# Kernel tuning notes

Measured on AMD Instinct MI355X. Metric: run time of the kernel, lower is better.

Reference implementation:

```python
import jax, jax.numpy as jnp
import numpy as np
import math

B, LQ, LK, DK, DV, H = 8, 2048, 2048, 128, 128, 8

def setup_inputs() -> dict:
    key = jax.random.key(0)
    ks = jax.random.split(key, 8)
    s = 0.02  # weight init scale
    return {
        "q": jax.random.normal(ks[0], (B, LQ, DK), jnp.float32),
        "k": jax.random.normal(ks[1], (B, LK, DK), jnp.float32),
        "v": jax.random.normal(ks[2], (B, LK, DV), jnp.float32),
        "Wq": jax.random.normal(ks[3], (DK, H * DK), jnp.float32) * s,
        "bq": jnp.zeros((H * DK,), jnp.float32),
        "Wk": jax.random.normal(ks[4], (DK, H * DK), jnp.float32) * s,
        "bk": jnp.zeros((H * DK,), jnp.float32),
        "Wv": jax.random.normal(ks[5], (DV, H * DV), jnp.float32) * s,
        "bv": jnp.zeros((H * DV,), jnp.float32),
        "Wo": jax.random.normal(ks[6], (H * DV, DV), jnp.float32) * s,
        "bo": jnp.zeros((DV,), jnp.float32),
    }

def reference(q, k, v, Wq, bq, Wk, bk, Wv, bv, Wo, bo):
    b, lq, dk = q.shape
    lk = k.shape[1]
    h = Wq.shape[1] // dk
    dv = Wv.shape[0]
    # projections -> [B, L, H, d]
    Qh = (q @ Wq + bq).reshape(b, lq, h, dk)
    Kh = (k @ Wk + bk).reshape(b, lk, h, dk)
    Vh = (v @ Wv + bv).reshape(b, lk, h, dv)
    scale = 1.0 / math.sqrt(dk)
    # full attention scores [B, H, Lq, Lk]
    scores = jnp.einsum("bqhd,bkhd->bhqk", Qh, Kh) * scale
    attn = jax.nn.softmax(scores, axis=-1)
    # dropout=0.0 in eval mode -> no-op
    out = jnp.einsum("bhqk,bkhd->bqhd", attn, Vh).reshape(b, lq, h * dv)
    return out @ Wo + bo  # [B, Lq, d_v]
```

## Files before the change

### kernel.cpp

```cpp
#include <hip/hip_runtime.h>
#include <hip/hip_bf16.h>
#include <math.h>


typedef __attribute__((ext_vector_type(8))) short s16x8;
typedef __attribute__((ext_vector_type(4))) short s16x4;
typedef __attribute__((ext_vector_type(4))) float f32x4;

#define MFMA16(a, b, c) __builtin_amdgcn_mfma_f32_16x16x32_bf16((a), (b), (c), 0, 0, 0)

static constexpr int HN = 8, LN = 2048;
static constexpr int MROWS = 16384;

static __device__ __forceinline__ unsigned short f2b(float f) {
  __hip_bfloat16 h = __float2bfloat16(f);
  union { __hip_bfloat16 h; unsigned short u; } cv;
  cv.h = h;
  return cv.u;
}

static __device__ __forceinline__ s16x8 ld16(const void* p) {
  uint4 t = *(const uint4*)p;
  return __builtin_bit_cast(s16x8, t);
}

static __device__ __forceinline__ void gload16(const void* g, void* l) {
  __builtin_amdgcn_global_load_lds(
      (const __attribute__((address_space(1))) unsigned int*)g,
      (__attribute__((address_space(3))) unsigned int*)l, 16, 0, 0);
}

static __device__ __forceinline__ unsigned cvt_pk(float lo, float hi) {
  unsigned r;
  asm("v_cvt_pk_bf16_f32 %0, %1, %2" : "=v"(r) : "v"(lo), "v"(hi));
  return r;
}

static __device__ __forceinline__ float fexp2(float x) {
  float r;
  asm("v_exp_f32 %0, %1" : "=v"(r) : "v"(x));
  return r;
}

__global__ __launch_bounds__(256) void cast_kernel(
    const float* __restrict__ q, const float* __restrict__ k,
    const float* __restrict__ v, const float* __restrict__ Wq,
    const float* __restrict__ Wk, const float* __restrict__ Wv,
    const float* __restrict__ Wo,
    __hip_bfloat16* __restrict__ qb, __hip_bfloat16* __restrict__ kb,
    __hip_bfloat16* __restrict__ vb, __hip_bfloat16* __restrict__ Wqt,
    __hip_bfloat16* __restrict__ Wkt, __hip_bfloat16* __restrict__ Wvt,
    __hip_bfloat16* __restrict__ Wot, float qscale)
{
  const int bid = blockIdx.x, tid = threadIdx.x;
  if (bid < 6144) {
    const int idx4 = bid * 256 + tid;
    const int arr  = idx4 >> 19;
    const int off4 = idx4 & ((1 << 19) - 1);
    const float* src = (arr == 0) ? q : (arr == 1) ? k : v;
    __hip_bfloat16* dst = (arr == 0) ? qb : (arr == 1) ? kb : vb;
    float4 ld = ((const float4*)src)[off4];
    s16x4 pk;
    pk[0] = (short)f2b(ld.x); pk[1] = (short)f2b(ld.y);
    pk[2] = (short)f2b(ld.z); pk[3] = (short)f2b(ld.w);
    ((s16x4*)dst)[off4] = pk;
  } else {
    const int t = (bid - 6144) * 256 + tid;
    const int which = t >> 17;
    const int i = t & ((1 << 17) - 1);
    if (which < 3) {
      const int n = i >> 7, kk = i & 127;
      const float* W = (which == 0) ? Wq : (which == 1) ? Wk : Wv;
      __hip_bfloat16* Wt = (which == 0) ? Wqt : (which == 1) ? Wkt : Wvt;
      float val = W[kk * 1024 + n];
      if (which == 0) val *= qscale;
      Wt[n * 128 + kk] = __float2bfloat16(val);
    } else {
      const int n = i >> 10, kk = i & 1023;
      Wot[n * 1024 + kk] = __float2bfloat16(Wo[kk * 128 + n]);
    }
  }
}

template <int MODE, int NF>
__global__ __launch_bounds__(256) void gemm_kernel(
    const __hip_bfloat16* __restrict__ A, const __hip_bfloat16* __restrict__ Btr,
    const float* __restrict__ bias, void* __restrict__ outp,
    int K, float bias_scale)
{
  constexpr int BUFB = (4 + NF) * 4096;
  __shared__ char lds[2 * BUFB];

  const int tid = threadIdx.x;
  const int l = tid & 63, w = tid >> 6;
  const int wr = w >> 1, wc = w & 1;
  const int m0 = blockIdx.x * 128, n0 = blockIdx.y * (NF * 32);
  const int cq = l & 15, rg = l >> 4;
  const int lrow8 = l >> 3, lcol8 = l & 7;
  const int swz8 = (lcol8 ^ lrow8) * 8;
  const int nk = K >> 6;

  f32x4 acc[4][NF] = {};

  auto stage = [&](int bb, int k0) {
    char* Ab = lds + bb * BUFB;
    char* Bb = Ab + 16384;
#pragma unroll
    for (int c = 0; c < 4; ++c) {
      const int ca = w * 4 + c;
      gload16(A + (size_t)(m0 + ca * 8 + lrow8) * K + k0 + swz8, Ab + ca * 1024);
    }
#pragma unroll
    for (int c = 0; c < NF; ++c) {
      const int cb = w * NF + c;
      gload16(Btr + (size_t)(n0 + cb * 8 + lrow8) * K + k0 + swz8, Bb + cb * 1024);
    }
  };

  stage(0, 0);
  __syncthreads();

  for (int kt = 0; kt < nk; ++kt) {
    const int cur = kt & 1;
    if (kt + 1 < nk) stage(cur ^ 1, (kt + 1) << 6);
    char* As = lds + cur * BUFB;
    char* Bs = As + 16384;
#pragma unroll
    for (int ks = 0; ks < 2; ++ks) {
      s16x8 af[4], bf[NF];
#pragma unroll
      for (int mf = 0; mf < 4; ++mf) {
        const int arow = wr * 64 + mf * 16 + cq;
        af[mf] = ld16(As + arow * 128 + ((ks * 64 + rg * 16) ^ ((arow & 7) << 4)));
      }
#pragma unroll
      for (int nf = 0; nf < NF; ++nf) {
        const int brow = wc * (NF * 16) + nf * 16 + cq;
        bf[nf] = ld16(Bs + brow * 128 + ((ks * 64 + rg * 16) ^ ((brow & 7) << 4)));
      }
#pragma unroll
      for (int mf = 0; mf < 4; ++mf)
#pragma unroll
        for (int nf = 0; nf < NF; ++nf)
          acc[mf][nf] = MFMA16(af[mf], bf[nf], acc[mf][nf]);
    }
    __syncthreads();
  }

#pragma unroll
  for (int nf = 0; nf < NF; ++nf) {
    const int gn = n0 + wc * (NF * 16) + nf * 16 + cq;
    const float bv = bias[gn] * bias_scale;
#pragma unroll
    for (int mf = 0; mf < 4; ++mf) {
      const int gm0 = m0 + wr * 64 + mf * 16 + rg * 4;
      const f32x4 a = acc[mf][nf];
      if (MODE == 0) {
        const int h = gn >> 7, d = gn & 127;
        __hip_bfloat16* o = (__hip_bfloat16*)outp;
#pragma unroll
        for (int r = 0; r < 4; ++r) {
          const int gm = gm0 + r;
          const int b = gm >> 11, lr = gm & (LN - 1);
          o[((size_t)(b * HN + h) * LN + lr) * 128 + d] = __float2bfloat16(a[r] + bv);
        }
      } else if (MODE == 2) {
        const int h = gn >> 7, d = gn & 127;
        const int b = gm0 >> 11, kv = gm0 & (LN - 1);
        s16x4 pk;
#pragma unroll
        for (int r = 0; r < 4; ++r) pk[r] = (short)f2b(a[r] + bv);
        *(s16x4*)((__hip_bfloat16*)outp + ((size_t)(b * HN + h) * 128 + d) * LN + kv) = pk;
      } else {
        float* o = (float*)outp;
#pragma unroll
        for (int r = 0; r < 4; ++r)
          o[(size_t)(gm0 + r) * 128 + gn] = a[r] + bv;
      }
    }
  }
}

__global__ __launch_bounds__(256, 2) void attn_kernel(
    const __hip_bfloat16* __restrict__ Qh, const __hip_bfloat16* __restrict__ Kh,
    const __hip_bfloat16* __restrict__ Vt, __hip_bfloat16* __restrict__ Obuf)
{
  __shared__ char lds[73728];
  char* Ks = lds;
  char* Vs = lds + 32768;

  const int x = blockIdx.x;
  const int xcd = x & 7, ii = x >> 3;
  const int bh = xcd * 8 + (ii >> 4);
  const int qt = ii & 15;

  const int tid = threadIdx.x, l = tid & 63, w = tid >> 6;
  const int cq = l & 15, rg = l >> 4;
  const int q0 = qt * 128 + w * 32;

  char* Pw = lds + 65536 + w * 2048;

  const char* Qc = (const char*)(Qh + (size_t)bh * LN * 128);
  const char* Kc = (const char*)(Kh + (size_t)bh * LN * 128);
  const char* Vc = (const char*)(Vt + (size_t)bh * 128 * LN);

  s16x8 qreg[2][4];
#pragma unroll
  for (int qf = 0; qf < 2; ++qf)
#pragma unroll
    for (int ks = 0; ks < 4; ++ks)
      qreg[qf][ks] = ld16(Qc + (size_t)(q0 + qf * 16 + cq) * 256 + ks * 64 + rg * 16);

  int kgoff[4], vgoff[4];
#pragma unroll
  for (int j = 0; j < 4; ++j) {
    const int ck = w * 256 + j * 64 + l;
    const int kr = ck >> 4, kc = ck & 15;
    kgoff[j] = kr * 256 + ((kc ^ (kr & 7)) * 16);
    const int vr = ck >> 3, vc = ck & 7;
    vgoff[j] = vr * 4096 + ((vc ^ (vr & 7)) * 16);
  }

  auto stageKV = [&](int buf, int t) {
    const char* kg = Kc + (size_t)t * 16384;
    const char* vg = Vc + (size_t)t * 128;
#pragma unroll
    for (int j = 0; j < 4; ++j) {
      gload16(kg + kgoff[j], Ks + buf * 16384 + w * 4096 + j * 1024);
      gload16(vg + vgoff[j], Vs + buf * 16384 + w * 4096 + j * 1024);
    }
  };

  f32x4 acc[8][2] = {};
  float ls0 = 0.f, ls1 = 0.f;

  stageKV(0, 0);
  __syncthreads();

#pragma unroll 2
  for (int t = 0; t < 32; ++t) {
    const int cur = t & 1;
    if (t < 31) stageKV(cur ^ 1, t + 1);
    char* Kb = Ks + cur * 16384;
    char* Vb = Vs + cur * 16384;

    f32x4 st[2][4] = {};
    __builtin_amdgcn_s_setprio(1);
#pragma unroll
    for (int t4 = 0; t4 < 4; ++t4) {
      const int row = t4 * 16 + cq;
      const int rsw = (row & 7) << 4;
      s16x8 kf[4];
#pragma unroll
      for (int ks = 0; ks < 4; ++ks)
        kf[ks] = ld16(Kb + row * 256 + ((ks * 64 + rg * 16) ^ rsw));
#pragma unroll
      for (int ks = 0; ks < 4; ++ks) {
        st[0][t4] = MFMA16(kf[ks], qreg[0][ks], st[0][t4]);
        st[1][t4] = MFMA16(kf[ks], qreg[1][ks], st[1][t4]);
      }
    }
    __builtin_amdgcn_s_setprio(0);

    s16x8 pb[2][2];
#pragma unroll
    for (int qf = 0; qf < 2; ++qf) {
      float sum = 0.f;
      const int prow = cq * 128;
      const int psw = (cq & 7) << 4;
#pragma unroll
      for (int t4 = 0; t4 < 4; ++t4) {
        const float e0 = fexp2(st[qf][t4][0]);
        const float e1 = fexp2(st[qf][t4][1]);
        const float e2 = fexp2(st[qf][t4][2]);
        const float e3 = fexp2(st[qf][t4][3]);
        sum += (e0 + e1) + (e2 + e3);
        uint2 pk;
        pk.x = cvt_pk(e0, e1);
        pk.y = cvt_pk(e2, e3);
        *(uint2*)(Pw + prow + ((t4 * 32 + rg * 8) ^ psw)) = pk;
      }
      if (qf) ls1 += sum; else ls0 += sum;
      pb[qf][0] = ld16(Pw + prow + ((rg * 16) ^ psw));
      pb[qf][1] = ld16(Pw + prow + ((64 + rg * 16) ^ psw));
    }

    __builtin_amdgcn_s_setprio(1);
#pragma unroll
    for (int fd = 0; fd < 8; ++fd) {
      const int vrow = fd * 16 + cq;
      const int vsw = (vrow & 7) << 4;
      s16x8 va0 = ld16(Vb + vrow * 128 + ((rg * 16) ^ vsw));
      s16x8 va1 = ld16(Vb + vrow * 128 + ((64 + rg * 16) ^ vsw));
      acc[fd][0] = MFMA16(va0, pb[0][0], acc[fd][0]);
      acc[fd][0] = MFMA16(va1, pb[0][1], acc[fd][0]);
      acc[fd][1] = MFMA16(va0, pb[1][0], acc[fd][1]);
      acc[fd][1] = MFMA16(va1, pb[1][1], acc[fd][1]);
    }
    __builtin_amdgcn_s_setprio(0);

    __syncthreads();
  }

  ls0 += __shfl_xor(ls0, 16); ls0 += __shfl_xor(ls0, 32);
  ls1 += __shfl_xor(ls1, 16); ls1 += __shfl_xor(ls1, 32);
  const float ri0 = 1.0f / ls0, ri1 = 1.0f / ls1;

  char* Ow = lds + w * 8192;
#pragma unroll
  for (int fd = 0; fd < 8; ++fd)
#pragma unroll
    for (int qf = 0; qf < 2; ++qf) {
      const float ri = qf ? ri1 : ri0;
      const int ql = qf * 16 + cq;
#pragma unroll
      for (int rr = 0; rr < 4; rr += 2) {
        const unsigned int pk = (unsigned)f2b(acc[fd][qf][rr] * ri) |
                                ((unsigned)f2b(acc[fd][qf][rr + 1] * ri) << 16);
        const int d0 = fd * 16 + rg * 4 + rr;
        *(unsigned int*)(Ow + ql * 256 + ((d0 * 2) ^ ((ql & 7) << 4))) = pk;
      }
    }
  const int b = bh >> 3, h = bh & 7;
#pragma unroll
  for (int pr = 0; pr < 8; ++pr) {
    const int ql = pr * 4 + rg;
    uint4 ov = *(const uint4*)(Ow + ql * 256 + ((cq * 16) ^ ((ql & 7) << 4)));
    *(uint4*)((char*)Obuf + ((size_t)(b * LN + q0 + ql) * 1024 + h * 128) * 2 + cq * 16) = ov;
  }
}

extern "C" void kernel_launch(void* const* d_in, const int* in_sizes, int n_in,
                              void* d_out, int out_size, void* d_ws, size_t ws_size,
                              hipStream_t stream)
{
  (void)in_sizes; (void)n_in; (void)out_size; (void)ws_size;
  const float* q  = (const float*)d_in[0];
  const float* k  = (const float*)d_in[1];
  const float* v  = (const float*)d_in[2];
  const float* Wq = (const float*)d_in[3];
  const float* bq = (const float*)d_in[4];
  const float* Wk = (const float*)d_in[5];
  const float* bk = (const float*)d_in[6];
  const float* Wv = (const float*)d_in[7];
  const float* bv = (const float*)d_in[8];
  const float* Wo = (const float*)d_in[9];
  const float* bo = (const float*)d_in[10];

  char* ws = (char*)d_ws;
  size_t off = 0;
  auto alloc = [&](size_t bytes) { char* p = ws + off; off += (bytes + 255) & ~(size_t)255; return p; };
  __hip_bfloat16* qb  = (__hip_bfloat16*)alloc((size_t)MROWS * 128 * 2);
  __hip_bfloat16* kb  = (__hip_bfloat16*)alloc((size_t)MROWS * 128 * 2);
  __hip_bfloat16* vb  = (__hip_bfloat16*)alloc((size_t)MROWS * 128 * 2);
  __hip_bfloat16* Wqt = (__hip_bfloat16*)alloc(1024 * 128 * 2);
  __hip_bfloat16* Wkt = (__hip_bfloat16*)alloc(1024 * 128 * 2);
  __hip_bfloat16* Wvt = (__hip_bfloat16*)alloc(1024 * 128 * 2);
  __hip_bfloat16* Wot = (__hip_bfloat16*)alloc(128 * 1024 * 2);
  __hip_bfloat16* Qh  = (__hip_bfloat16*)alloc((size_t)64 * LN * 128 * 2);
  __hip_bfloat16* Kh  = (__hip_bfloat16*)alloc((size_t)64 * LN * 128 * 2);
  __hip_bfloat16* Vt  = (__hip_bfloat16*)alloc((size_t)64 * LN * 128 * 2);
  __hip_bfloat16* Ob  = (__hip_bfloat16*)alloc((size_t)MROWS * 1024 * 2);

  const float qscale = 1.4426950408889634f / sqrtf(128.0f);

  cast_kernel<<<8192, 256, 0, stream>>>(q, k, v, Wq, Wk, Wv, Wo,
                                        qb, kb, vb, Wqt, Wkt, Wvt, Wot, qscale);
  gemm_kernel<0, 4><<<dim3(128, 8), 256, 0, stream>>>(qb, Wqt, bq, Qh, 128, qscale);
  gemm_kernel<0, 4><<<dim3(128, 8), 256, 0, stream>>>(kb, Wkt, bk, Kh, 128, 1.0f);
  gemm_kernel<2, 4><<<dim3(128, 8), 256, 0, stream>>>(vb, Wvt, bv, Vt, 128, 1.0f);
  attn_kernel<<<1024, 256, 0, stream>>>(Qh, Kh, Vt, Ob);
  gemm_kernel<3, 2><<<dim3(128, 2), 256, 0, stream>>>(Ob, Wot, bo, d_out, 1024, 1.0f);
}
```

Measured before the change: 216.3 us.

## Double attention Q tile per wave to 64 rows, halving grid

```diff
diff --git a/kernel.cpp b/kernel.cpp
--- a/kernel.cpp
+++ b/kernel.cpp
@@ -181,32 +181,32 @@
   }
 }
 
-__global__ __launch_bounds__(256, 2) void attn_kernel(
+__global__ __launch_bounds__(256, 1) void attn_kernel(
     const __hip_bfloat16* __restrict__ Qh, const __hip_bfloat16* __restrict__ Kh,
     const __hip_bfloat16* __restrict__ Vt, __hip_bfloat16* __restrict__ Obuf)
 {
-  __shared__ char lds[73728];
+  __shared__ char lds[98304];
   char* Ks = lds;
   char* Vs = lds + 32768;
 
   const int x = blockIdx.x;
   const int xcd = x & 7, ii = x >> 3;
-  const int bh = xcd * 8 + (ii >> 4);
-  const int qt = ii & 15;
+  const int bh = xcd * 8 + (ii >> 3);
+  const int qt = ii & 7;
 
   const int tid = threadIdx.x, l = tid & 63, w = tid >> 6;
   const int cq = l & 15, rg = l >> 4;
-  const int q0 = qt * 128 + w * 32;
-
-  char* Pw = lds + 65536 + w * 2048;
+  const int q0 = qt * 256 + w * 64;
+
+  char* Pw = lds + 65536 + w * 8192;
 
   const char* Qc = (const char*)(Qh + (size_t)bh * LN * 128);
   const char* Kc = (const char*)(Kh + (size_t)bh * LN * 128);
   const char* Vc = (const char*)(Vt + (size_t)bh * 128 * LN);
 
-  s16x8 qreg[2][4];
-#pragma unroll
-  for (int qf = 0; qf < 2; ++qf)
+  s16x8 qreg[4][4];
+#pragma unroll
+  for (int qf = 0; qf < 4; ++qf)
 #pragma unroll
     for (int ks = 0; ks < 4; ++ks)
       qreg[qf][ks] = ld16(Qc + (size_t)(q0 + qf * 16 + cq) * 256 + ks * 64 + rg * 16);
@@ -231,20 +231,21 @@
     }
   };
 
-  f32x4 acc[8][2] = {};
-  float ls0 = 0.f, ls1 = 0.f;
+  f32x4 acc[8][4] = {};
+  float ls[4] = {0.f, 0.f, 0.f, 0.f};
 
   stageKV(0, 0);
   __syncthreads();
 
-#pragma unroll 2
+  const int psw = (cq & 7) << 4;
+
   for (int t = 0; t < 32; ++t) {
     const int cur = t & 1;
     if (t < 31) stageKV(cur ^ 1, t + 1);
     char* Kb = Ks + cur * 16384;
     char* Vb = Vs + cur * 16384;
 
-    f32x4 st[2][4] = {};
+    f32x4 st[4][4] = {};
     __builtin_amdgcn_s_setprio(1);
 #pragma unroll
     for (int t4 = 0; t4 < 4; ++t4) {
@@ -255,19 +256,17 @@
       for (int ks = 0; ks < 4; ++ks)
         kf[ks] = ld16(Kb + row * 256 + ((ks * 64 + rg * 16) ^ rsw));
 #pragma unroll
-      for (int ks = 0; ks < 4; ++ks) {
-        st[0][t4] = MFMA16(kf[ks], qreg[0][ks], st[0][t4]);
-        st[1][t4] = MFMA16(kf[ks], qreg[1][ks], st[1][t4]);
-      }
+      for (int ks = 0; ks < 4; ++ks)
+#pragma unroll
+        for (int qf = 0; qf < 4; ++qf)
+          st[qf][t4] = MFMA16(kf[ks], qreg[qf][ks], st[qf][t4]);
     }
     __builtin_amdgcn_s_setprio(0);
 
-    s16x8 pb[2][2];
-#pragma unroll
-    for (int qf = 0; qf < 2; ++qf) {
+#pragma unroll
+    for (int qf = 0; qf < 4; ++qf) {
+      const int prow = (qf * 16 + cq) * 128;
       float sum = 0.f;
-      const int prow = cq * 128;
-      const int psw = (cq & 7) << 4;
 #pragma unroll
       for (int t4 = 0; t4 < 4; ++t4) {
         const float e0 = fexp2(st[qf][t4][0]);
@@ -280,7 +279,12 @@
         pk.y = cvt_pk(e2, e3);
         *(uint2*)(Pw + prow + ((t4 * 32 + rg * 8) ^ psw)) = pk;
       }
-      if (qf) ls1 += sum; else ls0 += sum;
+      ls[qf] += sum;
+    }
+    s16x8 pb[4][2];
+#pragma unroll
+    for (int qf = 0; qf < 4; ++qf) {
+      const int prow = (qf * 16 + cq) * 128;
       pb[qf][0] = ld16(Pw + prow + ((rg * 16) ^ psw));
       pb[qf][1] = ld16(Pw + prow + ((64 + rg * 16) ^ psw));
     }
@@ -292,38 +296,42 @@
       const int vsw = (vrow & 7) << 4;
       s16x8 va0 = ld16(Vb + vrow * 128 + ((rg * 16) ^ vsw));
       s16x8 va1 = ld16(Vb + vrow * 128 + ((64 + rg * 16) ^ vsw));
-      acc[fd][0] = MFMA16(va0, pb[0][0], acc[fd][0]);
-      acc[fd][0] = MFMA16(va1, pb[0][1], acc[fd][0]);
-      acc[fd][1] = MFMA16(va0, pb[1][0], acc[fd][1]);
-      acc[fd][1] = MFMA16(va1, pb[1][1], acc[fd][1]);
+#pragma unroll
+      for (int qf = 0; qf < 4; ++qf) {
+        acc[fd][qf] = MFMA16(va0, pb[qf][0], acc[fd][qf]);
+        acc[fd][qf] = MFMA16(va1, pb[qf][1], acc[fd][qf]);
+      }
     }
     __builtin_amdgcn_s_setprio(0);
 
     __syncthreads();
   }
 
-  ls0 += __shfl_xor(ls0, 16); ls0 += __shfl_xor(ls0, 32);
-  ls1 += __shfl_xor(ls1, 16); ls1 += __shfl_xor(ls1, 32);
-  const float ri0 = 1.0f / ls0, ri1 = 1.0f / ls1;
-
-  char* Ow = lds + w * 8192;
+  float ri[4];
+#pragma unroll
+  for (int qf = 0; qf < 4; ++qf) {
+    float s = ls[qf];
+    s += __shfl_xor(s, 16); s += __shfl_xor(s, 32);
+    ri[qf] = 1.0f / s;
+  }
+
+  char* Ow = lds + w * 16384;
 #pragma unroll
   for (int fd = 0; fd < 8; ++fd)
 #pragma unroll
-    for (int qf = 0; qf < 2; ++qf) {
-      const float ri = qf ? ri1 : ri0;
+    for (int qf = 0; qf < 4; ++qf) {
       const int ql = qf * 16 + cq;
 #pragma unroll
       for (int rr = 0; rr < 4; rr += 2) {
-        const unsigned int pk = (unsigned)f2b(acc[fd][qf][rr] * ri) |
-                                ((unsigned)f2b(acc[fd][qf][rr + 1] * ri) << 16);
+        const unsigned int pk = (unsigned)f2b(acc[fd][qf][rr] * ri[qf]) |
+                                ((unsigned)f2b(acc[fd][qf][rr + 1] * ri[qf]) << 16);
         const int d0 = fd * 16 + rg * 4 + rr;
         *(unsigned int*)(Ow + ql * 256 + ((d0 * 2) ^ ((ql & 7) << 4))) = pk;
       }
     }
   const int b = bh >> 3, h = bh & 7;
 #pragma unroll
-  for (int pr = 0; pr < 8; ++pr) {
+  for (int pr = 0; pr < 16; ++pr) {
     const int ql = pr * 4 + rg;
     uint4 ov = *(const uint4*)(Ow + ql * 256 + ((cq * 16) ^ ((ql & 7) << 4)));
     *(uint4*)((char*)Obuf + ((size_t)(b * LN + q0 + ql) * 1024 + h * 128) * 2 + cq * 16) = ov;
@@ -369,6 +377,6 @@
   gemm_kernel<0, 4><<<dim3(128, 8), 256, 0, stream>>>(qb, Wqt, bq, Qh, 128, qscale);
   gemm_kernel<0, 4><<<dim3(128, 8), 256, 0, stream>>>(kb, Wkt, bk, Kh, 128, 1.0f);
   gemm_kernel<2, 4><<<dim3(128, 8), 256, 0, stream>>>(vb, Wvt, bv, Vt, 128, 1.0f);
-  attn_kernel<<<1024, 256, 0, stream>>>(Qh, Kh, Vt, Ob);
+  attn_kernel<<<512, 256, 0, stream>>>(Qh, Kh, Vt, Ob);
   gemm_kernel<3, 2><<<dim3(128, 2), 256, 0, stream>>>(Ob, Wot, bo, d_out, 1024, 1.0f);
 }
```

Measured after the change: 266.8 us. 23.3% more time.

## Halve attention KV tile to 32 keys to shrink LDS footprint

Applied to the files above, without the earlier changes.

```diff
diff --git a/kernel.cpp b/kernel.cpp
--- a/kernel.cpp
+++ b/kernel.cpp
@@ -185,9 +185,9 @@
     const __hip_bfloat16* __restrict__ Qh, const __hip_bfloat16* __restrict__ Kh,
     const __hip_bfloat16* __restrict__ Vt, __hip_bfloat16* __restrict__ Obuf)
 {
-  __shared__ char lds[73728];
+  __shared__ char lds[40960];
   char* Ks = lds;
-  char* Vs = lds + 32768;
+  char* Vs = lds + 16384;
 
   const int x = blockIdx.x;
   const int xcd = x & 7, ii = x >> 3;
@@ -198,7 +198,7 @@
   const int cq = l & 15, rg = l >> 4;
   const int q0 = qt * 128 + w * 32;
 
-  char* Pw = lds + 65536 + w * 2048;
+  char* Pw = lds + 32768 + w * 2048;
 
   const char* Qc = (const char*)(Qh + (size_t)bh * LN * 128);
   const char* Kc = (const char*)(Kh + (size_t)bh * LN * 128);
@@ -211,23 +211,26 @@
     for (int ks = 0; ks < 4; ++ks)
       qreg[qf][ks] = ld16(Qc + (size_t)(q0 + qf * 16 + cq) * 256 + ks * 64 + rg * 16);
 
-  int kgoff[4], vgoff[4];
-#pragma unroll
-  for (int j = 0; j < 4; ++j) {
-    const int ck = w * 256 + j * 64 + l;
+  int kgoff[2], vgoff[2];
+#pragma unroll
+  for (int j = 0; j < 2; ++j) {
+    const int ck = w * 128 + j * 64 + l;
     const int kr = ck >> 4, kc = ck & 15;
     kgoff[j] = kr * 256 + ((kc ^ (kr & 7)) * 16);
-    const int vr = ck >> 3, vc = ck & 7;
-    vgoff[j] = vr * 4096 + ((vc ^ (vr & 7)) * 16);
+    const int vr = ck >> 3, vsl = ck & 7;
+    const int s2 = vsl ^ (vr & 7);
+    const int d  = vr * 2 + (s2 >> 2);
+    const int kvc = s2 & 3;
+    vgoff[j] = d * 4096 + kvc * 16;
   }
 
   auto stageKV = [&](int buf, int t) {
-    const char* kg = Kc + (size_t)t * 16384;
-    const char* vg = Vc + (size_t)t * 128;
-#pragma unroll
-    for (int j = 0; j < 4; ++j) {
-      gload16(kg + kgoff[j], Ks + buf * 16384 + w * 4096 + j * 1024);
-      gload16(vg + vgoff[j], Vs + buf * 16384 + w * 4096 + j * 1024);
+    const char* kg = Kc + (size_t)t * 8192;
+    const char* vg = Vc + (size_t)t * 64;
+#pragma unroll
+    for (int j = 0; j < 2; ++j) {
+      gload16(kg + kgoff[j], Ks + buf * 8192 + w * 2048 + j * 1024);
+      gload16(vg + vgoff[j], Vs + buf * 8192 + w * 2048 + j * 1024);
     }
   };
 
@@ -237,17 +240,18 @@
   stageKV(0, 0);
   __syncthreads();
 
-#pragma unroll 2
-  for (int t = 0; t < 32; ++t) {
+  const int cqs = cq & 3;
+
+  for (int t = 0; t < 64; ++t) {
     const int cur = t & 1;
-    if (t < 31) stageKV(cur ^ 1, t + 1);
-    char* Kb = Ks + cur * 16384;
-    char* Vb = Vs + cur * 16384;
-
-    f32x4 st[2][4] = {};
+    if (t < 63) stageKV(cur ^ 1, t + 1);
+    char* Kb = Ks + cur * 8192;
+    char* Vb = Vs + cur * 8192;
+
+    f32x4 st[2][2] = {};
     __builtin_amdgcn_s_setprio(1);
 #pragma unroll
-    for (int t4 = 0; t4 < 4; ++t4) {
+    for (int t4 = 0; t4 < 2; ++t4) {
       const int row = t4 * 16 + cq;
       const int rsw = (row & 7) << 4;
       s16x8 kf[4];
@@ -262,14 +266,13 @@
     }
     __builtin_amdgcn_s_setprio(0);
 
-    s16x8 pb[2][2];
+    s16x8 pb[2];
 #pragma unroll
     for (int qf = 0; qf < 2; ++qf) {
+      const int prow = (qf * 16 + cq) * 64;
       float sum = 0.f;
-      const int prow = cq * 128;
-      const int psw = (cq & 7) << 4;
-#pragma unroll
-      for (int t4 = 0; t4 < 4; ++t4) {
+#pragma unroll
+      for (int t4 = 0; t4 < 2; ++t4) {
         const float e0 = fexp2(st[qf][t4][0]);
         const float e1 = fexp2(st[qf][t4][1]);
         const float e2 = fexp2(st[qf][t4][2]);
@@ -278,24 +281,23 @@
         uint2 pk;
         pk.x = cvt_pk(e0, e1);
         pk.y = cvt_pk(e2, e3);
-        *(uint2*)(Pw + prow + ((t4 * 32 + rg * 8) ^ psw)) = pk;
+        const int byte = (((t4 * 2 + (rg >> 1)) ^ cqs) << 4) + ((rg & 1) * 8);
+        *(uint2*)(Pw + prow + byte) = pk;
       }
       if (qf) ls1 += sum; else ls0 += sum;
-      pb[qf][0] = ld16(Pw + prow + ((rg * 16) ^ psw));
-      pb[qf][1] = ld16(Pw + prow + ((64 + rg * 16) ^ psw));
+      pb[qf] = ld16(Pw + prow + ((rg ^ cqs) << 4));
     }
 
     __builtin_amdgcn_s_setprio(1);
 #pragma unroll
     for (int fd = 0; fd < 8; ++fd) {
       const int vrow = fd * 16 + cq;
-      const int vsw = (vrow & 7) << 4;
-      s16x8 va0 = ld16(Vb + vrow * 128 + ((rg * 16) ^ vsw));
-      s16x8 va1 = ld16(Vb + vrow * 128 + ((64 + rg * 16) ^ vsw));
-      acc[fd][0] = MFMA16(va0, pb[0][0], acc[fd][0]);
-      acc[fd][0] = MFMA16(va1, pb[0][1], acc[fd][0]);
-      acc[fd][1] = MFMA16(va0, pb[1][0], acc[fd][1]);
-      acc[fd][1] = MFMA16(va1, pb[1][1], acc[fd][1]);
+      const int r = vrow >> 1;
+      const int s2 = (vrow & 1) * 4 + rg;
+      const int s = s2 ^ (r & 7);
+      s16x8 va = ld16(Vb + r * 128 + (s << 4));
+      acc[fd][0] = MFMA16(va, pb[0], acc[fd][0]);
+      acc[fd][1] = MFMA16(va, pb[1], acc[fd][1]);
     }
     __builtin_amdgcn_s_setprio(0);
 
```

New measurement: 244.4 us. 1.13x slower.
